# Optimization experiments

Hardware: AMD Instinct MI355X
Metric: run time of the kernel (lower is better)

Reference implementation:

```python
import jax, jax.numpy as jnp
import numpy as np

K = 1024
D = 256
BETA = 0.25
DECAY = 0.99
EPS = 1e-05


def setup_inputs() -> dict:
    key = jax.random.key(0)
    k1, k2, k3, k4 = jax.random.split(key, 4)
    z_e = jax.random.normal(k1, (32, 2048, D), dtype=jnp.float32)
    emb = jax.random.normal(k2, (K, D), dtype=jnp.float32)
    # module L2-normalizes the codebook rows at init
    emb = emb / jnp.linalg.norm(emb, axis=1, keepdims=True)
    cluster_size = jax.random.uniform(k3, (K,), dtype=jnp.float32)
    embed_avg = jax.random.normal(k4, (K, D), dtype=jnp.float32)
    return {"z_e": z_e, "embedding": emb, "cluster_size": cluster_size, "embed_avg": embed_avg}


def reference(z_e, embedding, cluster_size, embed_avg):
    B, T, d = z_e.shape
    z = z_e.reshape(-1, d)                                   # [N, D]
    # squared-distance matrix: ||z||^2 - 2 z E^T + ||e||^2   -> [N, K]
    z_sq = jnp.sum(z * z, axis=1, keepdims=True)
    e_sq = jnp.sum(embedding * embedding, axis=1)[None, :]
    dist = z_sq - 2.0 * (z @ embedding.T) + e_sq
    codes = jnp.argmin(dist, axis=1)                         # [N]
    z_q = embedding[codes].reshape(z_e.shape)                # gather + reshape

    # ---- EMA codebook update (training branch, no-grad in torch) ----
    # scatter-reduce instead of materializing the [N, K] one-hot
    cs_batch = jax.ops.segment_sum(jnp.ones_like(codes, dtype=z.dtype), codes, num_segments=K)
    embed_sum = jax.ops.segment_sum(z, codes, num_segments=K)          # [K, D]
    new_cluster_size = cluster_size * DECAY + cs_batch * (1.0 - DECAY)
    new_embed_avg = embed_avg * DECAY + embed_sum * (1.0 - DECAY)
    n = jnp.sum(new_cluster_size)
    cs_smoothed = (new_cluster_size + EPS) / (n + K * EPS) * n
    new_embedding = new_embed_avg / cs_smoothed[:, None]

    commit_loss = jnp.mean((z_e - z_q) ** 2)
    vq_loss = BETA * commit_loss
    z_q_st = z_e + (z_q - z_e)  # straight-through (identical values in fwd)
    return (z_q_st, vq_loss, codes.reshape(B, T), new_embedding, new_cluster_size, new_embed_avg)
```

## Files before the change

### kernel.cpp

```cpp
#include <hip/hip_runtime.h>


#define DDIM 256
#define DQ   64
#define KC   1024
#define NROW 65536
#define BM   128
#define BN   128
#define BD   32
#define LS   34
#define DECAYF 0.99f
#define OMDF   0.01f
#define BETAF  0.25f
#define EPSF   1e-5f

#define BMR  128
#define NIT  24

typedef _Float16 f16;
typedef _Float16 f16x8 __attribute__((ext_vector_type(8)));
typedef float    f32x4 __attribute__((ext_vector_type(4)));

__device__ __forceinline__ void gl_lds16(const f16* g, f16* l) {
    __builtin_amdgcn_global_load_lds(
        (const __attribute__((address_space(1))) void*)g,
        (__attribute__((address_space(3))) void*)l, 16, 0, 0);
}

__global__ __launch_bounds__(256) void vq_esq(const float* __restrict__ emb,
                                              float* __restrict__ esq_g)
{
    int k = blockIdx.x * 256 + threadIdx.x;
    const float4* ep = (const float4*)(emb + (size_t)k * DDIM);
    float s = 0.f;
    for (int q = 0; q < DQ; ++q) {
        float4 v = ep[q];
        s += v.x * v.x + v.y * v.y + v.z * v.z + v.w * v.w;
    }
    esq_g[k] = s;
}

__global__ __launch_bounds__(256) void vq_prep(const float* __restrict__ src,
                                               f16* __restrict__ dst,
                                               float* __restrict__ sq_g)
{
    int t   = blockIdx.x * 256 + threadIdx.x;
    int row = t >> 5;
    int c   = t & 31;
    const float4* sp = (const float4*)(src + (size_t)row * DDIM + c * 8);
    float4 v0 = sp[0], v1 = sp[1];
    float x[8] = {v0.x, v0.y, v0.z, v0.w, v1.x, v1.y, v1.z, v1.w};
    f16x8 h, l;
    float s = 0.f;
#pragma unroll
    for (int j = 0; j < 8; ++j) {
        float xs = x[j] * 128.0f;
        f16 hh = (f16)xs;
        h[j] = hh;
        l[j] = (f16)(xs - (float)hh);
        s += x[j] * x[j];
    }
    f16* rp = dst + (size_t)row * 512;
    *(f16x8*)(rp + c * 8)       = h;
    *(f16x8*)(rp + 256 + c * 8) = l;
    s += __shfl_xor(s, 1);
    s += __shfl_xor(s, 2);
    s += __shfl_xor(s, 4);
    s += __shfl_xor(s, 8);
    s += __shfl_xor(s, 16);
    if (c == 0) sq_g[row] = s;
}

__global__ __launch_bounds__(256) void vq_prep_e(const float* __restrict__ emb,
                                                 f16* __restrict__ ehl2,
                                                 float* __restrict__ esq_g)
{
    int t     = blockIdx.x * 256 + threadIdx.x;
    int c     = t >> 5;
    int chunk = t & 31;
    const float4* sp = (const float4*)(emb + (size_t)c * DDIM + chunk * 8);
    float4 v0 = sp[0], v1 = sp[1];
    float x[8] = {v0.x, v0.y, v0.z, v0.w, v1.x, v1.y, v1.z, v1.w};
    f16x8 h, l;
    float s = 0.f;
#pragma unroll
    for (int j = 0; j < 8; ++j) {
        float xs = x[j] * 128.0f;
        f16 hh = (f16)xs;
        h[j] = hh;
        l[j] = (f16)(xs - (float)hh);
        s += x[j] * x[j];
    }
    int kb = chunk >> 2, kg = chunk & 3;
    int cg = c >> 4;
    int lanep = kg * 16 + (c & 15);
    size_t idx = ((size_t)(kb * 64 + cg)) * 512 + lanep * 8;
    *(f16x8*)(ehl2 + idx)          = h;
    *(f16x8*)(ehl2 + 262144 + idx) = l;
    s += __shfl_xor(s, 1);
    s += __shfl_xor(s, 2);
    s += __shfl_xor(s, 4);
    s += __shfl_xor(s, 8);
    s += __shfl_xor(s, 16);
    if (chunk == 0) esq_g[c] = s;
}


#define ASTAGE(b_, s_) do {                                                 \
    int off_ = (((s_) >= 8) ? 256 : 0) + ((s_) & 3) * 64;                   \
    gl_lds16(asrc0 + off_, &Abuf[b_][0] + tid * 8);                         \
    gl_lds16(asrc1 + off_, &Abuf[b_][0] + (tid + 512) * 8);                 \
} while (0)

#define BLOAD(dst_, it_, ks_) do {                                          \
    int itc_ = (it_) > NIT - 1 ? NIT - 1 : (it_);                           \
    int ps_ = itc_ / 12, sb_ = itc_ % 12;                                   \
    int pl_ = (sb_ >= 4 && sb_ < 8) ? 1 : 0;                                \
    int kb_ = (sb_ & 3) * 2 + (ks_);                                        \
    const f16* bp_ = ehl2 + (((size_t)((pl_ * 8 + kb_) * 64 + ps_ * 32      \
                   + wc * 4)) << 9) + lane * 8;                             \
    _Pragma("unroll")                                                       \
    for (int j_ = 0; j_ < 4; ++j_)                                          \
        dst_[j_] = *(const f16x8*)(bp_ + ((size_t)j_ << 9));                \
} while (0)

#define MM(bank_, Ab_, ks_) do {                                            \
    f16x8 a0_ = *(const f16x8*)((Ab_) + aoff[0][ks_]);                      \
    f16x8 a1_ = *(const f16x8*)((Ab_) + aoff[1][ks_]);                      \
    f16x8 a2_ = *(const f16x8*)((Ab_) + aoff[2][ks_]);                      \
    f16x8 a3_ = *(const f16x8*)((Ab_) + aoff[3][ks_]);                      \
    f16x8 a4_ = *(const f16x8*)((Ab_) + aoff[4][ks_]);                      \
    f16x8 a5_ = *(const f16x8*)((Ab_) + aoff[5][ks_]);                      \
    f16x8 a6_ = *(const f16x8*)((Ab_) + aoff[6][ks_]);                      \
    f16x8 a7_ = *(const f16x8*)((Ab_) + aoff[7][ks_]);                      \
    __builtin_amdgcn_s_setprio(1);                                          \
    _Pragma("unroll")                                                       \
    for (int j_ = 0; j_ < 4; ++j_) {                                        \
        acc[0][j_] = __builtin_amdgcn_mfma_f32_16x16x32_f16(a0_, bank_[j_], acc[0][j_], 0, 0, 0); \
        acc[1][j_] = __builtin_amdgcn_mfma_f32_16x16x32_f16(a1_, bank_[j_], acc[1][j_], 0, 0, 0); \
        acc[2][j_] = __builtin_amdgcn_mfma_f32_16x16x32_f16(a2_, bank_[j_], acc[2][j_], 0, 0, 0); \
        acc[3][j_] = __builtin_amdgcn_mfma_f32_16x16x32_f16(a3_, bank_[j_], acc[3][j_], 0, 0, 0); \
        acc[4][j_] = __builtin_amdgcn_mfma_f32_16x16x32_f16(a4_, bank_[j_], acc[4][j_], 0, 0, 0); \
        acc[5][j_] = __builtin_amdgcn_mfma_f32_16x16x32_f16(a5_, bank_[j_], acc[5][j_], 0, 0, 0); \
        acc[6][j_] = __builtin_amdgcn_mfma_f32_16x16x32_f16(a6_, bank_[j_], acc[6][j_], 0, 0, 0); \
        acc[7][j_] = __builtin_amdgcn_mfma_f32_16x16x32_f16(a7_, bank_[j_], acc[7][j_], 0, 0, 0); \
    }                                                                       \
    __builtin_amdgcn_s_setprio(0);                                          \
} while (0)

#define FOLD(P) do {                                                        \
    _Pragma("unroll")                                                       \
    for (int i_ = 0; i_ < 8; ++i_) {                                        \
      _Pragma("unroll")                                                     \
      for (int t_ = 0; t_ < 4; ++t_) {                                      \
        int row_ = i_ * 16 + kg * 4 + t_;                                   \
        float zq2_ = zsq_s[row_];                                           \
        float bv_ = 3.4e38f; int bix_ = 0;                                  \
        _Pragma("unroll")                                                   \
        for (int j_ = 0; j_ < 4; ++j_) {                                    \
          int col_ = (P) * 512 + wc * 64 + j_ * 16 + c16;                   \
          float d_ = fmaf(acc[i_][j_][t_], -0x1p-13f, zq2_) + esq_s[col_];  \
          if (d_ < bv_) { bv_ = d_; bix_ = col_; }                          \
        }                                                                   \
        _Pragma("unroll")                                                   \
        for (int m_ = 1; m_ < 16; m_ <<= 1) {                               \
          float ov_ = __shfl_xor(bv_, m_);                                  \
          int   oi_ = __shfl_xor(bix_, m_);                                 \
          if (ov_ < bv_ || (ov_ == bv_ && oi_ < bix_)) { bv_ = ov_; bix_ = oi_; } \
        }                                                                   \
        if (c16 == 0) {                                                     \
          red_v[((P) * 8 + wc) * 128 + row_] = bv_;                         \
          red_i[((P) * 8 + wc) * 128 + row_] = bix_;                        \
        }                                                                   \
      }                                                                     \
    }                                                                       \
    _Pragma("unroll")                                                       \
    for (int i_ = 0; i_ < 8; ++i_)                                          \
      _Pragma("unroll")                                                     \
      for (int j_ = 0; j_ < 4; ++j_) acc[i_][j_] = zero4;                   \
} while (0)

__global__ __launch_bounds__(512) void vq_main_mfma(
    const f16*  __restrict__ zhl,
    const f16*  __restrict__ ehl2,
    const float* __restrict__ esq_g,
    const float* __restrict__ zsq_g,
    float* __restrict__ out_codes)
{
    __shared__ f16   Abuf[2][8192];
    __shared__ float esq_s[KC];
    __shared__ float zsq_s[BMR];
    __shared__ float red_v[16 * BMR];
    __shared__ int   red_i[16 * BMR];

    const int tid  = threadIdx.x;
    const int row0 = blockIdx.x * BMR;
    const int wave = tid >> 6, lane = tid & 63;
    const int wc   = wave;
    const int kg   = lane >> 4, c16 = lane & 15;

    { float2 v = ((const float2*)esq_g)[tid];
      *(float2*)(esq_s + tid * 2) = v; }
    if (tid < BMR) zsq_s[tid] = zsq_g[row0 + tid];

    const int ar = tid >> 3, ach = tid & 7;
    const f16* asrc0 = zhl + (size_t)(row0 + ar) * 512 + (ach ^ (ar & 7)) * 8;
    const f16* asrc1 = asrc0 + (size_t)64 * 512;

    int aoff[8][2];
#pragma unroll
    for (int i = 0; i < 8; ++i)
#pragma unroll
        for (int ks = 0; ks < 2; ++ks)
            aoff[i][ks] = (i * 16 + c16) * 64
                        + (((ks * 4 + kg) ^ (c16 & 7)) * 8);

    f16x8 b0[4], b1[4];
    ASTAGE(0, 0);
    BLOAD(b0, 0, 0);
    asm volatile("s_waitcnt vmcnt(0) lgkmcnt(0)" ::: "memory");
    __builtin_amdgcn_s_barrier();

    f32x4 acc[8][4];
    const f32x4 zero4 = {0.f, 0.f, 0.f, 0.f};
#pragma unroll
    for (int i = 0; i < 8; ++i)
#pragma unroll
        for (int j = 0; j < 4; ++j) acc[i][j] = zero4;

#pragma unroll 1
    for (int it = 0; it < NIT; ++it) {
        const f16* Ab = &Abuf[it & 1][0];
        if (it < NIT - 1) {
            int its = it + 1;
            ASTAGE(its & 1, its % 12);
        }
        __builtin_amdgcn_sched_barrier(0);
        BLOAD(b1, it, 1);
        MM(b0, Ab, 0);
        BLOAD(b0, it + 1, 0);
        MM(b1, Ab, 1);
        if ((it % 12) == 11) { FOLD(it / 12); }
        asm volatile("s_waitcnt vmcnt(8)" ::: "memory");
        __builtin_amdgcn_s_barrier();
    }

    __syncthreads();
    if (tid < BMR) {
        float bv = red_v[tid];
        int   bi = red_i[tid];
#pragma unroll
        for (int t = 1; t < 16; ++t) {
            float v  = red_v[t * 128 + tid];
            int   ix = red_i[t * 128 + tid];
            if (v < bv || (v == bv && ix < bi)) { bv = v; bi = ix; }
        }
        out_codes[row0 + tid] = (float)bi;
    }
}

__global__ __launch_bounds__(256) void vq_epi(
    const float* __restrict__ z,
    const float* __restrict__ emb,
    const float* __restrict__ codes_f,
    float* __restrict__ out_zq,
    float* __restrict__ loss_acc)
{
    __shared__ int   codes_s[64];
    __shared__ float lred[256];
    const int tid  = threadIdx.x;
    const int row0 = blockIdx.x * 64;
    const int wave = tid >> 6, lane = tid & 63;

    if (tid < 64) codes_s[tid] = (int)codes_f[row0 + tid];
    __syncthreads();

    float lp = 0.f;
#pragma unroll 1
    for (int r = wave; r < 64; r += 4) {
        int code = codes_s[r];
        float4 e4 = *(const float4*)(emb + (size_t)code * DDIM + lane * 4);
        float4 z4 = *(const float4*)(z + (size_t)(row0 + r) * DDIM + lane * 4);
        float dx = e4.x - z4.x, dy = e4.y - z4.y, dz = e4.z - z4.z, dw = e4.w - z4.w;
        float4 o;
        o.x = z4.x + dx; o.y = z4.y + dy; o.z = z4.z + dz; o.w = z4.w + dw;
        *(float4*)(out_zq + (size_t)(row0 + r) * DDIM + lane * 4) = o;
        lp += dx * dx + dy * dy + dz * dz + dw * dw;
    }
    lred[tid] = lp;
    __syncthreads();
    for (int s = 128; s > 0; s >>= 1) {
        if (tid < s) lred[tid] += lred[tid + s];
        __syncthreads();
    }
    if (tid == 0) atomicAdd(loss_acc, lred[0]);
}

__global__ __launch_bounds__(256) void vq_main_f32(
    const float* __restrict__ z,
    const float* __restrict__ emb,
    const float* __restrict__ esq_g,
    float* __restrict__ out_zq,
    float* __restrict__ out_codes,
    float* __restrict__ loss_acc)
{
    __shared__ float zs[BM * LS];
    __shared__ float es[BN * LS];
    __shared__ float esq_s[KC];
    __shared__ float zsq_s[BM];
    float* red_v   = zs;
    int*   red_i   = (int*)(zs + 2048);
    int*   codes_s = (int*)es;
    float* lred    = es + 128;

    const int tid  = threadIdx.x;
    const int row0 = blockIdx.x * BM;
    const int trow = tid >> 4;
    const int tcol = tid & 15;

    {
        const float4* eg = (const float4*)esq_g;
        float4 v = eg[tid];
        *(float4*)(esq_s + tid * 4) = v;
    }
    if (tid < BM) {
        const float4* zp = (const float4*)(z + (size_t)(row0 + tid) * DDIM);
        float s = 0.f;
        for (int q = 0; q < DQ; ++q) {
            float4 v = zp[q];
            s += v.x * v.x + v.y * v.y + v.z * v.z + v.w * v.w;
        }
        zsq_s[tid] = s;
    }

    const int r0 = tid >> 3;
    const int q0 = tid & 7;
    const float* zp0 = z + (size_t)(row0 + r0) * DDIM + q0 * 4;
    const float* ep0 = emb + (size_t)r0 * DDIM + q0 * 4;
    const int ls0 = r0 * LS + q0 * 4;

    float4 pz[4], pe[4];
#pragma unroll
    for (int it = 0; it < 4; ++it) {
        pz[it] = *(const float4*)(zp0 + it * 32 * DDIM);
        pe[it] = *(const float4*)(ep0 + it * 32 * DDIM);
    }

    float runv[8];
    int   runi[8];
#pragma unroll
    for (int i = 0; i < 8; ++i) { runv[i] = 3.4e38f; runi[i] = 0; }

#pragma unroll 1
    for (int kt = 0; kt < KC / BN; ++kt) {
        float acc[8][8];
#pragma unroll
        for (int i = 0; i < 8; ++i)
#pragma unroll
            for (int j = 0; j < 8; ++j) acc[i][j] = 0.f;

#pragma unroll 1
        for (int dc = 0; dc < DDIM / BD; ++dc) {
            __syncthreads();
#pragma unroll
            for (int it = 0; it < 4; ++it) {
                int o = ls0 + it * 32 * LS;
                *(float2*)(zs + o)     = make_float2(pz[it].x, pz[it].y);
                *(float2*)(zs + o + 2) = make_float2(pz[it].z, pz[it].w);
                *(float2*)(es + o)     = make_float2(pe[it].x, pe[it].y);
                *(float2*)(es + o + 2) = make_float2(pe[it].z, pe[it].w);
            }
            __syncthreads();
            {
                int ndc = dc + 1, nkt = kt;
                if (ndc == DDIM / BD) { ndc = 0; ++nkt; }
                if (nkt < KC / BN) {
                    size_t zo = (size_t)ndc * BD;
                    size_t eo = (size_t)nkt * BN * DDIM + (size_t)ndc * BD;
#pragma unroll
                    for (int it = 0; it < 4; ++it) {
                        pz[it] = *(const float4*)(zp0 + it * 32 * DDIM + zo);
                        pe[it] = *(const float4*)(ep0 + it * 32 * DDIM + eo);
                    }
                }
            }
#pragma unroll
            for (int s = 0; s < BD / 2; ++s) {
                float2 a2[8], b2[8];
#pragma unroll
                for (int i = 0; i < 8; ++i)
                    a2[i] = *(const float2*)(zs + (trow + 16 * i) * LS + s * 2);
#pragma unroll
                for (int j = 0; j < 8; ++j)
                    b2[j] = *(const float2*)(es + (tcol + 16 * j) * LS + s * 2);
#pragma unroll
                for (int i = 0; i < 8; ++i)
#pragma unroll
                    for (int j = 0; j < 8; ++j)
                        acc[i][j] = fmaf(a2[i].y, b2[j].y,
                                     fmaf(a2[i].x, b2[j].x, acc[i][j]));
            }
        }
#pragma unroll
        for (int i = 0; i < 8; ++i) {
            float zq2 = zsq_s[trow + 16 * i];
#pragma unroll
            for (int j = 0; j < 8; ++j) {
                int col = kt * BN + tcol + 16 * j;
                float dist = zq2 - 2.f * acc[i][j] + esq_s[col];
                if (dist < runv[i]) { runv[i] = dist; runi[i] = col; }
            }
        }
    }

    __syncthreads();
#pragma unroll
    for (int i = 0; i < 8; ++i) {
        int lr = trow + 16 * i;
        red_v[lr * 16 + tcol] = runv[i];
        red_i[lr * 16 + tcol] = runi[i];
    }
    __syncthreads();
    if (tid < BM) {
        float bv = red_v[tid * 16];
        int   bi = red_i[tid * 16];
        for (int t = 1; t < 16; ++t) {
            float v  = red_v[tid * 16 + t];
            int   ix = red_i[tid * 16 + t];
            if (v < bv || (v == bv && ix < bi)) { bv = v; bi = ix; }
        }
        codes_s[tid] = bi;
        out_codes[row0 + tid] = (float)bi;
    }
    __syncthreads();

    const int wavf = tid >> 6;
    const int lanf = tid & 63;
    float lp = 0.f;
    for (int r = wavf; r < BM; r += 4) {
        int code = codes_s[r];
        float4 e4 = *(const float4*)(emb + (size_t)code * DDIM + lanf * 4);
        float4 z4 = *(const float4*)(z + (size_t)(row0 + r) * DDIM + lanf * 4);
        float dx = e4.x - z4.x, dy = e4.y - z4.y, dz = e4.z - z4.z, dw = e4.w - z4.w;
        float4 o;
        o.x = z4.x + dx; o.y = z4.y + dy; o.z = z4.z + dz; o.w = z4.w + dw;
        *(float4*)(out_zq + (size_t)(row0 + r) * DDIM + lanf * 4) = o;
        lp += dx * dx + dy * dy + dz * dz + dw * dw;
    }
    lred[tid] = lp;
    __syncthreads();
    for (int s = 128; s > 0; s >>= 1) {
        if (tid < s) lred[tid] += lred[tid + s];
        __syncthreads();
    }
    if (tid == 0) atomicAdd(loss_acc, lred[0]);
}

__global__ __launch_bounds__(256) void vq_scatter(
    const float* __restrict__ z,
    const float* __restrict__ codes_f,
    float* __restrict__ embed_sum,
    float* __restrict__ counts)
{
    __shared__ int list[1024];
    __shared__ int nmatch;
    const int k   = blockIdx.x;
    const int tid = threadIdx.x;

    float acc = 0.f;
    int total = 0;
    if (tid == 0) nmatch = 0;
    __syncthreads();

    for (int base = 0; base < NROW; base += 1024) {
        float4 c4 = *(const float4*)(codes_f + base + tid * 4);
        int i0 = base + tid * 4;
        if ((int)c4.x == k) { int p = atomicAdd(&nmatch, 1); list[p] = i0; }
        if ((int)c4.y == k) { int p = atomicAdd(&nmatch, 1); list[p] = i0 + 1; }
        if ((int)c4.z == k) { int p = atomicAdd(&nmatch, 1); list[p] = i0 + 2; }
        if ((int)c4.w == k) { int p = atomicAdd(&nmatch, 1); list[p] = i0 + 3; }
        __syncthreads();
        int nm = nmatch;
        for (int i = 0; i < nm; ++i)
            acc += z[(size_t)list[i] * DDIM + tid];
        total += nm;
        __syncthreads();
        if (tid == 0) nmatch = 0;
        __syncthreads();
    }
    embed_sum[(size_t)k * DDIM + tid] = acc;
    if (tid == 0) counts[k] = (float)total;
}

__global__ void vq_finalize(const float* __restrict__ cluster_size,
                            const float* __restrict__ counts,
                            const float* __restrict__ loss_acc,
                            float* __restrict__ out_ncs,
                            float* __restrict__ out_loss,
                            float* __restrict__ cs_sm,
                            float inv_ND)
{
    __shared__ float sred[KC];
    const int tid = threadIdx.x;
    float ncs = cluster_size[tid] * DECAYF + counts[tid] * OMDF;
    out_ncs[tid] = ncs;
    sred[tid] = ncs;
    __syncthreads();
    for (int s = KC / 2; s > 0; s >>= 1) {
        if (tid < s) sred[tid] += sred[tid + s];
        __syncthreads();
    }
    float n = sred[0];
    cs_sm[tid] = (ncs + EPSF) / (n + (float)KC * EPSF) * n;
    if (tid == 0) out_loss[0] = BETAF * loss_acc[0] * inv_ND;
}

__global__ void vq_embed(const float* __restrict__ embed_avg,
                         const float* __restrict__ embed_sum,
                         const float* __restrict__ cs_sm,
                         float* __restrict__ out_nea,
                         float* __restrict__ out_nemb)
{
    int idx = blockIdx.x * blockDim.x + threadIdx.x;
    int k = idx >> 6;
    float4 ea = ((const float4*)embed_avg)[idx];
    float4 s4 = ((const float4*)embed_sum)[idx];
    float4 nea;
    nea.x = ea.x * DECAYF + s4.x * OMDF;
    nea.y = ea.y * DECAYF + s4.y * OMDF;
    nea.z = ea.z * DECAYF + s4.z * OMDF;
    nea.w = ea.w * DECAYF + s4.w * OMDF;
    ((float4*)out_nea)[idx] = nea;
    float cs = cs_sm[k];
    float4 ne;
    ne.x = nea.x / cs; ne.y = nea.y / cs; ne.z = nea.z / cs; ne.w = nea.w / cs;
    ((float4*)out_nemb)[idx] = ne;
}

extern "C" void kernel_launch(void* const* d_in, const int* in_sizes, int n_in,
                              void* d_out, int out_size, void* d_ws, size_t ws_size,
                              hipStream_t stream) {
    const float* z            = (const float*)d_in[0];
    const float* emb          = (const float*)d_in[1];
    const float* cluster_size = (const float*)d_in[2];
    const float* embed_avg    = (const float*)d_in[3];

    const int ND = in_sizes[0];
    const int KD = in_sizes[1];
    const int K  = in_sizes[2];
    const int N  = ND / DDIM;

    float* out       = (float*)d_out;
    float* out_zq    = out;
    float* out_loss  = out + (size_t)ND;
    float* out_codes = out + (size_t)ND + 1;
    float* out_nemb  = out + (size_t)ND + 1 + N;
    float* out_ncs   = out_nemb + (size_t)KD;
    float* out_nea   = out_ncs + (size_t)K;

    float* ws        = (float*)d_ws;
    float* loss_acc  = ws;
    float* counts    = ws + 1;
    float* cs_sm     = counts + K;
    float* esq_g     = cs_sm + K;
    float* zsq_g     = esq_g + K;
    float* embed_sum = zsq_g + N;

    size_t base_floats = (size_t)1 + 3 * (size_t)K + (size_t)N + (size_t)KD;
    size_t f16_off = (base_floats * sizeof(float) + 255) & ~(size_t)255;
    size_t zbytes  = (size_t)N * 512 * sizeof(f16);
    size_t ebytes  = (size_t)2 * 262144 * sizeof(f16);
    bool mfma_ok   = ws_size >= f16_off + zbytes + ebytes;

    hipMemsetAsync(loss_acc, 0, sizeof(float), stream);
    if (mfma_ok) {
        f16* zhl  = (f16*)((char*)d_ws + f16_off);
        f16* ehl2 = (f16*)((char*)d_ws + f16_off + zbytes);
        vq_prep<<<(N * 32) / 256, 256, 0, stream>>>(z, zhl, zsq_g);
        vq_prep_e<<<(K * 32) / 256, 256, 0, stream>>>(emb, ehl2, esq_g);
        vq_main_mfma<<<N / BMR, 512, 0, stream>>>(
            zhl, ehl2, esq_g, zsq_g, out_codes);
        vq_epi<<<N / 64, 256, 0, stream>>>(z, emb, out_codes, out_zq, loss_acc);
    } else {
        vq_esq<<<K / 256, 256, 0, stream>>>(emb, esq_g);
        vq_main_f32<<<N / BM, 256, 0, stream>>>(z, emb, esq_g,
                                                out_zq, out_codes, loss_acc);
    }
    vq_scatter<<<K, 256, 0, stream>>>(z, out_codes, embed_sum, counts);
    vq_finalize<<<1, K, 0, stream>>>(cluster_size, counts, loss_acc,
                                     out_ncs, out_loss, cs_sm, 1.0f / (float)ND);
    vq_embed<<<KD / 1024, 256, 0, stream>>>(embed_avg, embed_sum, cs_sm,
                                            out_nea, out_nemb);
}
```

Measured before the change: 365.2 us.

## Halve MFMA row tile to 64 with 4 waves and simplify load pipeline

Shrinks the main distance/argmin kernel from 128-row, 512-thread blocks to 64-row, 256-thread blocks, doubling the number of codebook passes and blocks. Accumulator and A-operand register usage halves, which may raise occupancy. The software-pipelined B prefetch with manual waitcnt/barrier is replaced by loading B at the start of each iteration and using __syncthreads. This risks exposing global load latency and doubles codebook traffic per row.

```diff
diff --git a/kernel.cpp b/kernel.cpp
--- a/kernel.cpp
+++ b/kernel.cpp
@@ -14,8 +14,8 @@
 #define BETAF  0.25f
 #define EPSF   1e-5f
 
-#define BMR  128
-#define NIT  24
+#define BMR  64
+#define NIT  48
 
 typedef _Float16 f16;
 typedef _Float16 f16x8 __attribute__((ext_vector_type(8)));
@@ -109,15 +109,13 @@
 #define ASTAGE(b_, s_) do {                                                 \
     int off_ = (((s_) >= 8) ? 256 : 0) + ((s_) & 3) * 64;                   \
     gl_lds16(asrc0 + off_, &Abuf[b_][0] + tid * 8);                         \
-    gl_lds16(asrc1 + off_, &Abuf[b_][0] + (tid + 512) * 8);                 \
+    gl_lds16(asrc1 + off_, &Abuf[b_][0] + (tid + 256) * 8);                 \
 } while (0)
 
-#define BLOAD(dst_, it_, ks_) do {                                          \
-    int itc_ = (it_) > NIT - 1 ? NIT - 1 : (it_);                           \
-    int ps_ = itc_ / 12, sb_ = itc_ % 12;                                   \
-    int pl_ = (sb_ >= 4 && sb_ < 8) ? 1 : 0;                                \
-    int kb_ = (sb_ & 3) * 2 + (ks_);                                        \
-    const f16* bp_ = ehl2 + (((size_t)((pl_ * 8 + kb_) * 64 + ps_ * 32      \
+#define BLOAD(dst_, p_, sb_, ks_) do {                                      \
+    int pl_ = ((sb_) >= 4 && (sb_) < 8) ? 1 : 0;                            \
+    int kb_ = ((sb_) & 3) * 2 + (ks_);                                      \
+    const f16* bp_ = ehl2 + (((size_t)((pl_ * 8 + kb_) * 64 + (p_) * 16     \
                    + wc * 4)) << 9) + lane * 8;                             \
     _Pragma("unroll")                                                       \
     for (int j_ = 0; j_ < 4; ++j_)                                          \
@@ -129,10 +127,6 @@
     f16x8 a1_ = *(const f16x8*)((Ab_) + aoff[1][ks_]);                      \
     f16x8 a2_ = *(const f16x8*)((Ab_) + aoff[2][ks_]);                      \
     f16x8 a3_ = *(const f16x8*)((Ab_) + aoff[3][ks_]);                      \
-    f16x8 a4_ = *(const f16x8*)((Ab_) + aoff[4][ks_]);                      \
-    f16x8 a5_ = *(const f16x8*)((Ab_) + aoff[5][ks_]);                      \
-    f16x8 a6_ = *(const f16x8*)((Ab_) + aoff[6][ks_]);                      \
-    f16x8 a7_ = *(const f16x8*)((Ab_) + aoff[7][ks_]);                      \
     __builtin_amdgcn_s_setprio(1);                                          \
     _Pragma("unroll")                                                       \
     for (int j_ = 0; j_ < 4; ++j_) {                                        \
@@ -140,17 +134,13 @@
         acc[1][j_] = __builtin_amdgcn_mfma_f32_16x16x32_f16(a1_, bank_[j_], acc[1][j_], 0, 0, 0); \
         acc[2][j_] = __builtin_amdgcn_mfma_f32_16x16x32_f16(a2_, bank_[j_], acc[2][j_], 0, 0, 0); \
         acc[3][j_] = __builtin_amdgcn_mfma_f32_16x16x32_f16(a3_, bank_[j_], acc[3][j_], 0, 0, 0); \
-        acc[4][j_] = __builtin_amdgcn_mfma_f32_16x16x32_f16(a4_, bank_[j_], acc[4][j_], 0, 0, 0); \
-        acc[5][j_] = __builtin_amdgcn_mfma_f32_16x16x32_f16(a5_, bank_[j_], acc[5][j_], 0, 0, 0); \
-        acc[6][j_] = __builtin_amdgcn_mfma_f32_16x16x32_f16(a6_, bank_[j_], acc[6][j_], 0, 0, 0); \
-        acc[7][j_] = __builtin_amdgcn_mfma_f32_16x16x32_f16(a7_, bank_[j_], acc[7][j_], 0, 0, 0); \
     }                                                                       \
     __builtin_amdgcn_s_setprio(0);                                          \
 } while (0)
 
 #define FOLD(P) do {                                                        \
     _Pragma("unroll")                                                       \
-    for (int i_ = 0; i_ < 8; ++i_) {                                        \
+    for (int i_ = 0; i_ < 4; ++i_) {                                        \
       _Pragma("unroll")                                                     \
       for (int t_ = 0; t_ < 4; ++t_) {                                      \
         int row_ = i_ * 16 + kg * 4 + t_;                                   \
@@ -158,7 +148,7 @@
         float bv_ = 3.4e38f; int bix_ = 0;                                  \
         _Pragma("unroll")                                                   \
         for (int j_ = 0; j_ < 4; ++j_) {                                    \
-          int col_ = (P) * 512 + wc * 64 + j_ * 16 + c16;                   \
+          int col_ = (P) * 256 + wc * 64 + j_ * 16 + c16;                   \
           float d_ = fmaf(acc[i_][j_][t_], -0x1p-13f, zq2_) + esq_s[col_];  \
           if (d_ < bv_) { bv_ = d_; bix_ = col_; }                          \
         }                                                                   \
@@ -169,25 +159,25 @@
           if (ov_ < bv_ || (ov_ == bv_ && oi_ < bix_)) { bv_ = ov_; bix_ = oi_; } \
         }                                                                   \
         if (c16 == 0) {                                                     \
-          red_v[((P) * 8 + wc) * 128 + row_] = bv_;                         \
-          red_i[((P) * 8 + wc) * 128 + row_] = bix_;                        \
+          red_v[((P) * 4 + wc) * BMR + row_] = bv_;                         \
+          red_i[((P) * 4 + wc) * BMR + row_] = bix_;                        \
         }                                                                   \
       }                                                                     \
     }                                                                       \
     _Pragma("unroll")                                                       \
-    for (int i_ = 0; i_ < 8; ++i_)                                          \
+    for (int i_ = 0; i_ < 4; ++i_)                                          \
       _Pragma("unroll")                                                     \
       for (int j_ = 0; j_ < 4; ++j_) acc[i_][j_] = zero4;                   \
 } while (0)
 
-__global__ __launch_bounds__(512) void vq_main_mfma(
+__global__ __launch_bounds__(256) void vq_main_mfma(
     const f16*  __restrict__ zhl,
     const f16*  __restrict__ ehl2,
     const float* __restrict__ esq_g,
     const float* __restrict__ zsq_g,
     float* __restrict__ out_codes)
 {
-    __shared__ f16   Abuf[2][8192];
+    __shared__ f16   Abuf[2][4096];
     __shared__ float esq_s[KC];
     __shared__ float zsq_s[BMR];
     __shared__ float red_v[16 * BMR];
@@ -199,60 +189,56 @@
     const int wc   = wave;
     const int kg   = lane >> 4, c16 = lane & 15;
 
-    { float2 v = ((const float2*)esq_g)[tid];
-      *(float2*)(esq_s + tid * 2) = v; }
+    { float4 v = ((const float4*)esq_g)[tid];
+      *(float4*)(esq_s + tid * 4) = v; }
     if (tid < BMR) zsq_s[tid] = zsq_g[row0 + tid];
 
     const int ar = tid >> 3, ach = tid & 7;
     const f16* asrc0 = zhl + (size_t)(row0 + ar) * 512 + (ach ^ (ar & 7)) * 8;
-    const f16* asrc1 = asrc0 + (size_t)64 * 512;
-
-    int aoff[8][2];
-#pragma unroll
-    for (int i = 0; i < 8; ++i)
+    const f16* asrc1 = asrc0 + (size_t)32 * 512;
+
+    int aoff[4][2];
+#pragma unroll
+    for (int i = 0; i < 4; ++i)
 #pragma unroll
         for (int ks = 0; ks < 2; ++ks)
             aoff[i][ks] = (i * 16 + c16) * 64
                         + (((ks * 4 + kg) ^ (c16 & 7)) * 8);
 
+    ASTAGE(0, 0);
+    __syncthreads();
+
+    f32x4 acc[4][4];
+    const f32x4 zero4 = {0.f, 0.f, 0.f, 0.f};
+#pragma unroll
+    for (int i = 0; i < 4; ++i)
+#pragma unroll
+        for (int j = 0; j < 4; ++j) acc[i][j] = zero4;
+
     f16x8 b0[4], b1[4];
-    ASTAGE(0, 0);
-    BLOAD(b0, 0, 0);
-    asm volatile("s_waitcnt vmcnt(0) lgkmcnt(0)" ::: "memory");
-    __builtin_amdgcn_s_barrier();
-
-    f32x4 acc[8][4];
-    const f32x4 zero4 = {0.f, 0.f, 0.f, 0.f};
-#pragma unroll
-    for (int i = 0; i < 8; ++i)
-#pragma unroll
-        for (int j = 0; j < 4; ++j) acc[i][j] = zero4;
-
+    int sb = 0, p = 0;
 #pragma unroll 1
     for (int it = 0; it < NIT; ++it) {
         const f16* Ab = &Abuf[it & 1][0];
-        if (it < NIT - 1) {
-            int its = it + 1;
-            ASTAGE(its & 1, its % 12);
+        BLOAD(b0, p, sb, 0);
+        BLOAD(b1, p, sb, 1);
+        if (it + 1 < NIT) {
+            int sn = sb + 1 == 12 ? 0 : sb + 1;
+            ASTAGE((it + 1) & 1, sn);
         }
-        __builtin_amdgcn_sched_barrier(0);
-        BLOAD(b1, it, 1);
         MM(b0, Ab, 0);
-        BLOAD(b0, it + 1, 0);
         MM(b1, Ab, 1);
-        if ((it % 12) == 11) { FOLD(it / 12); }
-        asm volatile("s_waitcnt vmcnt(8)" ::: "memory");
-        __builtin_amdgcn_s_barrier();
-    }
-
-    __syncthreads();
+        if (sb == 11) { FOLD(p); sb = 0; ++p; } else { ++sb; }
+        __syncthreads();
+    }
+
     if (tid < BMR) {
         float bv = red_v[tid];
         int   bi = red_i[tid];
 #pragma unroll
         for (int t = 1; t < 16; ++t) {
-            float v  = red_v[t * 128 + tid];
-            int   ix = red_i[t * 128 + tid];
+            float v  = red_v[t * BMR + tid];
+            int   ix = red_i[t * BMR + tid];
             if (v < bv || (v == bv && ix < bi)) { bv = v; bi = ix; }
         }
         out_codes[row0 + tid] = (float)bi;
@@ -578,7 +564,7 @@
         f16* ehl2 = (f16*)((char*)d_ws + f16_off + zbytes);
         vq_prep<<<(N * 32) / 256, 256, 0, stream>>>(z, zhl, zsq_g);
         vq_prep_e<<<(K * 32) / 256, 256, 0, stream>>>(emb, ehl2, esq_g);
-        vq_main_mfma<<<N / BMR, 512, 0, stream>>>(
+        vq_main_mfma<<<N / BMR, 256, 0, stream>>>(
             zhl, ehl2, esq_g, zsq_g, out_codes);
         vq_epi<<<N / 64, 256, 0, stream>>>(z, emb, out_codes, out_zq, loss_acc);
     } else {
```

Measured after the change: 410.6 us. 1.12x slower.
